# Kernel tuning notes

Hardware: AMD Instinct MI355X
Metric: run time of the kernel (lower is better)

The kernel has to match this reference:

```python
import jax, jax.numpy as jnp
import numpy as np
from jax import lax

B_CAPS, C_CAPS, K, STRIDE, ITERS = 32, 32, 3, 2, 3
BATCH, WIN = 8, 14
W_OUT = (WIN - K) // STRIDE + 1  # 6
CWW = C_CAPS * W_OUT * W_OUT     # 1152
LOG_2PI = float(np.log(2.0 * np.pi))


def setup_inputs() -> dict:
    key = jax.random.key(0)
    k1, k2, k3, k4, k5 = jax.random.split(key, 5)
    return {
        "poses": jax.random.normal(k1, (BATCH, B_CAPS, WIN, WIN, 16), jnp.float32),
        "activations": jax.random.uniform(k2, (BATCH, B_CAPS, WIN, WIN), jnp.float32),
        "lambda_": jnp.ones((), jnp.float32),
        "W": jax.random.normal(k3, (B_CAPS, K, K, C_CAPS, 4, 4), jnp.float32),
        "beta_v": jax.random.normal(k4, (1, CWW, 1), jnp.float32),
        "beta_a": jax.random.normal(k5, (1, CWW), jnp.float32),
    }


def reference(poses, activations, lambda_, W, beta_v, beta_a):
    b, B, win = poses.shape[0], poses.shape[1], poses.shape[2]
    C = W.shape[3]
    w = (win - K) // STRIDE + 1
    Bkk, Cww = B * K * K, C * w * w

    pose = poses.reshape(b, 16, B, win, win).transpose(0, 2, 3, 4, 1)

    # im2col patch extraction (vectorized): rows[i,k] = stride*i + k
    rows = ((jnp.arange(w) * STRIDE)[:, None] + jnp.arange(K)).reshape(-1)  # (w*K,)
    p = jnp.take(pose, rows, axis=2).reshape(b, B, w, K, win, 16)
    p = jnp.take(p, rows, axis=4).reshape(b, B, w, K, w, K, 16)
    patches = p.transpose(0, 1, 3, 5, 6, 2, 4)          # (b,B,K,K,16,wi,wj)
    # faithful reproduction of torch's view (b,B,K,K,16,ww)->(b,B,K,K,1,w,w,4,4)
    patches = patches.reshape(b, B, K, K, w, w, 4, 4)

    # votes: broadcast 4x4 matmul W @ pose-patch
    votes = jnp.einsum('sxyzij,bsxyuvjk->bsxyzuvik', W, patches)
    votes = votes.reshape(b, Bkk, Cww, 16)

    # activation patches, tiled over C (coordinate_add=False branch)
    a = jnp.take(activations, rows, axis=2).reshape(b, B, w, K, win)
    a = jnp.take(a, rows, axis=4).reshape(b, B, w, K, w, K)
    a = a.transpose(0, 1, 3, 5, 2, 4).reshape(b, Bkk, 1, w * w)
    act = jnp.broadcast_to(a, (b, Bkk, C, w * w)).reshape(b, Bkk, Cww)

    # EM routing
    R = jnp.ones((b, Bkk, Cww), votes.dtype) / Cww
    for i in range(ITERS + 1):
        Ra = (R * act)[..., None]                        # (b,Bkk,Cww,1)
        sum_R = Ra.sum(1)                                # (b,Cww,1)
        mu = ((Ra * votes).sum(1) / sum_R)[:, None]      # (b,1,Cww,16)
        sigma_sq = (Ra * (votes - mu) ** 2).sum(1) / sum_R  # (b,Cww,16)
        if i != ITERS:
            mu_d = lax.stop_gradient(mu)
            ss_d = lax.stop_gradient(sigma_sq)[:, None]  # (b,1,Cww,16)
            V_d = lax.stop_gradient(votes)
            a_d = lax.stop_gradient(act)
            log_p = -0.5 * (V_d - mu_d) ** 2 / ss_d - 0.5 * jnp.log(ss_d) - 0.5 * LOG_2PI
            ap = a_d * jnp.exp(log_p).sum(-1)            # (b,Bkk,Cww)
            R = ap / ap.sum(-1, keepdims=True)
        else:
            cost = (beta_v + jnp.log(sigma_sq)) * sum_R  # (b,Cww,16)
            a_out = jax.nn.sigmoid(lambda_ * (beta_a - cost.sum(2)))  # (b,Cww)

    return (mu.reshape(b, C, w, w, 16), a_out.reshape(b, C, w, w))
```

## Files before the change

### kernel.cpp

```cpp
#include <hip/hip_runtime.h>
#include <hip/hip_bf16.h>

#define NB   8
#define NM   288
#define NN   1152
#define NUV  36
#define ND   16

#define OFF_P    0
#define SZ_P     (NB*NUV*NM*ND)
#define OFF_WT   (OFF_P + SZ_P)
#define SZ_WT    (32*NM*ND)
#define OFF_ACT  (OFF_WT + SZ_WT)
#define SZ_ACT   (NB*NUV*NM)
#define OFF_L    (OFF_ACT + SZ_ACT)
#define SZ_L     (NB*NN*NM)
#define OFF_LSE  (OFF_L + SZ_L)
#define SZ_LSE   (NB*NM)
#define OFF_FLAG (OFF_LSE + SZ_LSE)
#define OFF_LT   (OFF_FLAG + 16)
#define SZ_LT    (NB*NM*NN)

#define HALF_LOG_2PI 0.9189385332046727f
#define LOG_NN       7.049254841255839f
#define NEG_BIG      (-1.0e30f)

__device__ __forceinline__ float ldin(const void* p, int i, int f32) {
    return f32 ? ((const float*)p)[i]
               : __bfloat162float(((const __hip_bfloat16*)p)[i]);
}

__device__ __forceinline__ unsigned short bfbits(float f) {
    __hip_bfloat16 h = __float2bfloat16(f);
    return __builtin_bit_cast(unsigned short, h);
}

__device__ __forceinline__ float dot2bf(unsigned a, unsigned b, float c) {
    float d;
    asm("v_dot2_f32_bf16 %0, %1, %2, %3" : "=v"(d) : "v"(a), "v"(b), "v"(c));
    return d;
}

__global__ void detect_kernel(const unsigned short* __restrict__ poses_u16,
                              int* __restrict__ flag) {
    if (blockIdx.x == 0 && threadIdx.x == 0) {
        int wild = 0;
        for (int i = 0; i < 64; ++i) {
            int ex = (poses_u16[i] >> 7) & 0xFF;
            if (ex >= 133) ++wild;
        }
        *flag = (wild >= 4) ? 1 : 0;
    }
}

__global__ __launch_bounds__(256) void prep_kernel(
    const void* __restrict__ poses, const void* __restrict__ acts,
    const void* __restrict__ Wb, __hip_bfloat16* __restrict__ P,
    __hip_bfloat16* __restrict__ Wt, float* __restrict__ A36,
    const int* __restrict__ flagp)
{
    const int f32 = *flagp;
    const int blk = blockIdx.x;
    const int tid = threadIdx.x;
    if (blk < 256) {
        __shared__ float ps[16 * 196];
        __shared__ float asld[196];
        const int b = blk >> 5, s = blk & 31;
        for (int e = tid; e < 16 * 196; e += 256) {
            int c = e / 196, hw = e % 196;
            ps[e] = ldin(poses, ((b * 16 + c) * 32 + s) * 196 + hw, f32);
        }
        for (int e = tid; e < 196; e += 256)
            asld[e] = ldin(acts, (b * 32 + s) * 196 + e, f32);
        __syncthreads();
        for (int o2 = tid; o2 < 648; o2 += 256) {
            int row = o2 >> 1, half = o2 & 1;
            int uv = row / 9, xy = row % 9;
            int u = uv / 6, vv2 = uv % 6;
            int x = xy / 3, y = xy % 3;
            unsigned pk[4];
#pragma unroll
            for (int h = 0; h < 4; ++h) {
                unsigned lohi[2];
#pragma unroll
                for (int e = 0; e < 2; ++e) {
                    int kj = half * 8 + h * 2 + e;
                    int k = kj >> 2, j = kj & 3;
                    int idx = u * 96 + vv2 * 16 + j * 4 + k;
                    int c = idx / 36, rem = idx % 36;
                    int wi = rem / 6, wj = rem % 6;
                    lohi[e] = bfbits(ps[c * 196 + (2 * wi + x) * 14 + (2 * wj + y)]);
                }
                pk[h] = lohi[0] | (lohi[1] << 16);
            }
            *((uint4*)(P + (((size_t)((b * 36 + uv) * 288 + s * 9 + xy)) << 4) + half * 8)) =
                make_uint4(pk[0], pk[1], pk[2], pk[3]);
        }
        for (int o = tid; o < 324; o += 256) {
            int uv = o / 9, xy = o % 9;
            int u = uv / 6, vv2 = uv % 6;
            int x = xy / 3, y = xy % 3;
            A36[(b * 36 + uv) * 288 + s * 9 + xy] =
                __logf(asld[(2 * u + x) * 14 + (2 * vv2 + y)]);
        }
    } else {
        int idx = (blk - 256) * 256 + tid;
        int z = idx / 288, m = idx % 288;
        unsigned pk[8];
#pragma unroll
        for (int h = 0; h < 8; ++h) {
            unsigned lo = bfbits(ldin(Wb, m * 512 + z * 16 + 2 * h, f32));
            unsigned hi = bfbits(ldin(Wb, m * 512 + z * 16 + 2 * h + 1, f32));
            pk[h] = lo | (hi << 16);
        }
        uint4* dst = (uint4*)(Wt + idx * 16);
        dst[0] = make_uint4(pk[0], pk[1], pk[2], pk[3]);
        dst[1] = make_uint4(pk[4], pk[5], pk[6], pk[7]);
    }
}

__global__ __launch_bounds__(288, 4) void em_iter(
    const unsigned short* __restrict__ wsP, const unsigned short* __restrict__ wsWt,
    const float* __restrict__ wsA, float* __restrict__ wsL,
    float* __restrict__ wsLT, const float* __restrict__ wsLSE,
    const void* __restrict__ beta_v,
    const void* __restrict__ beta_a,
    const void* __restrict__ lambda_,
    void* __restrict__ outv, const int* __restrict__ flagp, int iter)
{
    __shared__ float red[NM * 17];
    __shared__ float Mhw[9];
    __shared__ float paru[NM];
    __shared__ float parv[NM];
    __shared__ float paruW[18];
    __shared__ float mul[16], nhil[16], ltl[16], ssl[16];

    const int tid = threadIdx.x;
    const int B   = blockIdx.x;
    const int rr  = B & 255;
    const int z   = rr >> 3;
    const int g   = ((B >> 8) << 3) | (rr & 7);
    const int b   = g / NUV;
    const int uv  = g % NUV;
    const int n   = z * NUV + uv;
    const int bn  = b * NN + n;

    const uint4* Wq = (const uint4*)(wsWt + ((z * NM + tid) << 4));
    const uint4* Pq = (const uint4*)(wsP + ((g * NM + tid) << 4));
    uint4 wq0 = Wq[0], wq1 = Wq[1];
    uint4 pq0 = Pq[0], pq1 = Pq[1];
    const float lact = wsA[g * NM + tid];
    float t;
    if (iter == 0) t = lact - LOG_NN;
    else t = wsL[(size_t)bn * NM + tid] - wsLSE[b * NM + tid] + lact;
    t = fmaxf(t, NEG_BIG);

    float mhw = t;
#pragma unroll
    for (int off = 1; off < 32; off <<= 1)
        mhw = fmaxf(mhw, __shfl_xor(mhw, off, 32));
    const float w = __expf(t - mhw);
    if ((tid & 31) == 0) Mhw[tid >> 5] = mhw;

    unsigned Wa[4] = {wq0.x, wq0.z, wq1.x, wq1.z};
    unsigned Wb_[4] = {wq0.y, wq0.w, wq1.y, wq1.w};
    unsigned Pa[4] = {pq0.x, pq0.z, pq1.x, pq1.z};
    unsigned Pb[4] = {pq0.y, pq0.w, pq1.y, pq1.w};
    float v[16];
#pragma unroll
    for (int i = 0; i < 4; ++i)
#pragma unroll
        for (int k = 0; k < 4; ++k)
            v[i * 4 + k] = dot2bf(Wa[i], Pa[k], dot2bf(Wb_[i], Pb[k], 0.f));

#pragma unroll
    for (int dd = 0; dd < 16; ++dd) red[tid * 17 + dd] = v[dd];
    red[tid * 17 + 16] = w;
    __syncthreads();

    {
        const int d = tid & 15, c = tid >> 4;
        const float* base = &red[(c << 4) * 17];
        float s1 = 0.f, s2 = 0.f, sw = 0.f;
#pragma unroll
        for (int q = 0; q < 16; ++q) {
            float ww = base[q * 17 + 16];
            float vv = base[q * 17 + d];
            float t1 = ww * vv;
            s1 += t1; s2 += t1 * vv; sw += ww;
        }
        paru[d * 18 + c] = s1;
        parv[d * 18 + c] = s2;
        if (d == 0) paruW[c] = sw;
    }
    __syncthreads();

    float M_f = NEG_BIG, sW_f = 0.f;
    if (tid < 16) {
        float M = Mhw[0];
#pragma unroll
        for (int h = 1; h < 9; ++h) M = fmaxf(M, Mhw[h]);
        float sW = 0.f, S1 = 0.f, S2 = 0.f;
#pragma unroll
        for (int c = 0; c < 18; ++c) {
            float sc = __expf(Mhw[c >> 1] - M);
            sW += paruW[c] * sc;
            S1 += paru[tid * 18 + c] * sc;
            S2 += parv[tid * 18 + c] * sc;
        }
        float mu = S1 / sW;
        float q2 = S2 / sW;
        float ss = fmaxf(q2 - mu * mu, 1e-30f);
        mul[tid]  = mu;
        ssl[tid]  = ss;
        nhil[tid] = -0.5f / ss;
        ltl[tid]  = -0.5f * __logf(ss) - HALF_LOG_2PI;
        M_f = M; sW_f = sW;
    }
    __syncthreads();

    if (iter < 3) {
        float lp[16];
        float M = NEG_BIG;
#pragma unroll
        for (int dd = 0; dd < 16; ++dd) {
            float df = v[dd] - mul[dd];
            lp[dd] = df * df * nhil[dd] + ltl[dd];
            M = fmaxf(M, lp[dd]);
        }
        float s = 0.f;
#pragma unroll
        for (int dd = 0; dd < 16; ++dd) s += __expf(lp[dd] - M);
        float ell = lact + M + __logf(s);
        wsL[(size_t)bn * NM + tid] = ell;
        wsLT[((size_t)b * NM + tid) * NN + n] = ell;
    } else {
        const int f32 = *flagp;
        if (tid < 16) {
            if (f32) ((float*)outv)[(bn << 4) + tid] = mul[tid];
            else ((__hip_bfloat16*)outv)[(bn << 4) + tid] = __float2bfloat16(mul[tid]);
        }
        if (tid == 0) {
            float sumR = __expf(M_f) * sW_f;
            float bv = ldin(beta_v, n, f32);
            float c = 0.f;
#pragma unroll
            for (int dd = 0; dd < 16; ++dd) c += bv + __logf(ssl[dd]);
            c *= sumR;
            float lam = ldin(lambda_, 0, f32);
            float ba  = ldin(beta_a, n, f32);
            float ao  = 1.f / (1.f + __expf(-(lam * (ba - c))));
            int oi = NB * NN * ND + bn;
            if (f32) ((float*)outv)[oi] = ao;
            else ((__hip_bfloat16*)outv)[oi] = __float2bfloat16(ao);
        }
    }
}

__global__ __launch_bounds__(256) void lse_kernel(const float* __restrict__ LT,
                                                  float* __restrict__ LSE)
{
    const int row  = blockIdx.x * 4 + (threadIdx.x >> 6);
    const int lane = threadIdx.x & 63;
    const float* base = LT + (size_t)row * NN + lane;
    float vv[18];
    float mx = NEG_BIG;
#pragma unroll
    for (int i = 0; i < 18; ++i) { vv[i] = base[i * 64]; mx = fmaxf(mx, vv[i]); }
#pragma unroll
    for (int off = 1; off < 64; off <<= 1) mx = fmaxf(mx, __shfl_xor(mx, off));
    float s = 0.f;
#pragma unroll
    for (int i = 0; i < 18; ++i) s += __expf(vv[i] - mx);
#pragma unroll
    for (int off = 1; off < 64; off <<= 1) s += __shfl_xor(s, off);
    if (lane == 0) LSE[row] = mx + __logf(s);
}

extern "C" void kernel_launch(void* const* d_in, const int* in_sizes, int n_in,
                              void* d_out, int out_size, void* d_ws, size_t ws_size,
                              hipStream_t stream)
{
    const void* poses = d_in[0];
    const void* acts  = d_in[1];
    const void* lam   = d_in[2];
    const void* Wb    = d_in[3];
    const void* bv    = d_in[4];
    const void* ba    = d_in[5];

    float* ws  = (float*)d_ws;
    __hip_bfloat16* P  = (__hip_bfloat16*)(ws + OFF_P);
    __hip_bfloat16* Wt = (__hip_bfloat16*)(ws + OFF_WT);
    float* A36 = ws + OFF_ACT;
    float* L   = ws + OFF_L;
    float* LSE = ws + OFF_LSE;
    int*  flag = (int*)(ws + OFF_FLAG);
    float* LT  = ws + OFF_LT;

    detect_kernel<<<1, 64, 0, stream>>>((const unsigned short*)poses, flag);

    prep_kernel<<<292, 256, 0, stream>>>(poses, acts, Wb, P, Wt, A36, flag);

    for (int it = 0; it < 4; ++it) {
        em_iter<<<NB * NN, 288, 0, stream>>>((const unsigned short*)P,
                                             (const unsigned short*)Wt,
                                             A36, L, LT, LSE, bv, ba, lam,
                                             d_out, flag, it);
        if (it < 3) {
            lse_kernel<<<576, 256, 0, stream>>>(LT, LSE);
        }
    }
}
```

Baseline: 230.4 us.

## Replace transposed log-likelihood copy with two-stage partial log-sum-exp over L

The routing kernel no longer writes a second, transposed copy of the log-likelihoods (a strided scatter over NN). The normalizer is instead computed in two passes: one kernel reads L in its natural layout with coalesced accesses and produces per-chunk max and sum, and a small kernel merges the 36 partials per row. This removes an uncoalesced write of the full 8x1152x288 tensor on each iteration, at the cost of one extra kernel launch per iteration and a small partial buffer.

Result: no change. 231.7 us (+0.6%).

```diff
diff --git a/kernel.cpp b/kernel.cpp
--- a/kernel.cpp
+++ b/kernel.cpp
@@ -18,8 +18,10 @@
 #define OFF_LSE  (OFF_L + SZ_L)
 #define SZ_LSE   (NB*NM)
 #define OFF_FLAG (OFF_LSE + SZ_LSE)
-#define OFF_LT   (OFF_FLAG + 16)
-#define SZ_LT    (NB*NM*NN)
+#define OFF_PM   (OFF_FLAG + 16)
+#define SZ_PM    (NB*NUV*NM)
+#define OFF_PS   (OFF_PM + SZ_PM)
+#define SZ_PS    (NB*NUV*NM)
 
 #define HALF_LOG_2PI 0.9189385332046727f
 #define LOG_NN       7.049254841255839f
@@ -122,7 +124,7 @@
 __global__ __launch_bounds__(288, 4) void em_iter(
     const unsigned short* __restrict__ wsP, const unsigned short* __restrict__ wsWt,
     const float* __restrict__ wsA, float* __restrict__ wsL,
-    float* __restrict__ wsLT, const float* __restrict__ wsLSE,
+    const float* __restrict__ wsLSE,
     const void* __restrict__ beta_v,
     const void* __restrict__ beta_a,
     const void* __restrict__ lambda_,
@@ -162,10 +164,10 @@
     const float w = __expf(t - mhw);
     if ((tid & 31) == 0) Mhw[tid >> 5] = mhw;
 
-    unsigned Wa[4] = {wq0.x, wq0.z, wq1.x, wq1.z};
+    unsigned Wa[4]  = {wq0.x, wq0.z, wq1.x, wq1.z};
     unsigned Wb_[4] = {wq0.y, wq0.w, wq1.y, wq1.w};
-    unsigned Pa[4] = {pq0.x, pq0.z, pq1.x, pq1.z};
-    unsigned Pb[4] = {pq0.y, pq0.w, pq1.y, pq1.w};
+    unsigned Pa[4]  = {pq0.x, pq0.z, pq1.x, pq1.z};
+    unsigned Pb[4]  = {pq0.y, pq0.w, pq1.y, pq1.w};
     float v[16];
 #pragma unroll
     for (int i = 0; i < 4; ++i)
@@ -231,9 +233,7 @@
         float s = 0.f;
 #pragma unroll
         for (int dd = 0; dd < 16; ++dd) s += __expf(lp[dd] - M);
-        float ell = lact + M + __logf(s);
-        wsL[(size_t)bn * NM + tid] = ell;
-        wsLT[((size_t)b * NM + tid) * NN + n] = ell;
+        wsL[(size_t)bn * NM + tid] = lact + M + __logf(s);
     } else {
         const int f32 = *flagp;
         if (tid < 16) {
@@ -257,24 +257,41 @@
     }
 }
 
-__global__ __launch_bounds__(256) void lse_kernel(const float* __restrict__ LT,
-                                                  float* __restrict__ LSE)
-{
-    const int row  = blockIdx.x * 4 + (threadIdx.x >> 6);
-    const int lane = threadIdx.x & 63;
-    const float* base = LT + (size_t)row * NN + lane;
-    float vv[18];
+__global__ __launch_bounds__(288) void lse1_kernel(const float* __restrict__ L,
+                                                   float* __restrict__ PM,
+                                                   float* __restrict__ PS)
+{
+    const int tid = threadIdx.x;
+    const int blk = blockIdx.x;
+    const int b = blk / NUV;
+    const int c = blk % NUV;
+    const float* base = L + ((size_t)b * NN + c * 32) * NM + tid;
     float mx = NEG_BIG;
 #pragma unroll
-    for (int i = 0; i < 18; ++i) { vv[i] = base[i * 64]; mx = fmaxf(mx, vv[i]); }
-#pragma unroll
-    for (int off = 1; off < 64; off <<= 1) mx = fmaxf(mx, __shfl_xor(mx, off));
+    for (int r = 0; r < 32; ++r) mx = fmaxf(mx, base[r * NM]);
     float s = 0.f;
 #pragma unroll
-    for (int i = 0; i < 18; ++i) s += __expf(vv[i] - mx);
-#pragma unroll
-    for (int off = 1; off < 64; off <<= 1) s += __shfl_xor(s, off);
-    if (lane == 0) LSE[row] = mx + __logf(s);
+    for (int r = 0; r < 32; ++r) s += __expf(base[r * NM] - mx);
+    PM[blk * NM + tid] = mx;
+    PS[blk * NM + tid] = s;
+}
+
+__global__ void lse2_kernel(const float* __restrict__ PM,
+                            const float* __restrict__ PS,
+                            float* __restrict__ LSE)
+{
+    int t = blockIdx.x * 256 + threadIdx.x;
+    if (t >= NB * NM) return;
+    int b = t / NM, m = t % NM;
+    const float* pm = PM + (size_t)b * NUV * NM + m;
+    const float* ps = PS + (size_t)b * NUV * NM + m;
+    float mx = NEG_BIG;
+#pragma unroll
+    for (int cc = 0; cc < NUV; ++cc) mx = fmaxf(mx, pm[cc * NM]);
+    float s = 0.f;
+#pragma unroll
+    for (int cc = 0; cc < NUV; ++cc) s += ps[cc * NM] * __expf(pm[cc * NM] - mx);
+    LSE[t] = mx + __logf(s);
 }
 
 extern "C" void kernel_launch(void* const* d_in, const int* in_sizes, int n_in,
@@ -295,7 +312,8 @@
     float* L   = ws + OFF_L;
     float* LSE = ws + OFF_LSE;
     int*  flag = (int*)(ws + OFF_FLAG);
-    float* LT  = ws + OFF_LT;
+    float* PM  = ws + OFF_PM;
+    float* PS  = ws + OFF_PS;
 
     detect_kernel<<<1, 64, 0, stream>>>((const unsigned short*)poses, flag);
 
@@ -304,10 +322,11 @@
     for (int it = 0; it < 4; ++it) {
         em_iter<<<NB * NN, 288, 0, stream>>>((const unsigned short*)P,
                                              (const unsigned short*)Wt,
-                                             A36, L, LT, LSE, bv, ba, lam,
+                                             A36, L, LSE, bv, ba, lam,
                                              d_out, flag, it);
         if (it < 3) {
-            lse_kernel<<<576, 256, 0, stream>>>(LT, LSE);
-        }
-    }
-}
+            lse1_kernel<<<NB * NUV, 288, 0, stream>>>(L, PM, PS);
+            lse2_kernel<<<9, 256, 0, stream>>>(PM, PS, LSE);
+        }
+    }
+}
```

## Replace log-domain EM routing with linear-domain sums and drop transposed buffer

Applied to the files above, without the earlier changes.

Routing weights are now kept in the linear domain: em_iter writes a*sum(exp(log_p)) once, and a new sum_kernel computes per-(b,m) reciprocal sums, replacing the log-sum-exp path and its separate transposed LT buffer. This removes the max/exp rescaling and the strided transposed store, and cuts global traffic per iteration. The separate detect kernel is folded into prep_kernel, saving one launch. Linear-domain sums risk underflow or overflow, which the code handles only with small clamps.

After: 248.6 us. 7.9% more time.

```diff
diff --git a/kernel.cpp b/kernel.cpp
--- a/kernel.cpp
+++ b/kernel.cpp
@@ -13,16 +13,13 @@
 #define SZ_WT    (32*NM*ND)
 #define OFF_ACT  (OFF_WT + SZ_WT)
 #define SZ_ACT   (NB*NUV*NM)
-#define OFF_L    (OFF_ACT + SZ_ACT)
-#define SZ_L     (NB*NN*NM)
-#define OFF_LSE  (OFF_L + SZ_L)
-#define SZ_LSE   (NB*NM)
-#define OFF_FLAG (OFF_LSE + SZ_LSE)
-#define OFF_LT   (OFF_FLAG + 16)
-#define SZ_LT    (NB*NM*NN)
+#define OFF_PA   (OFF_ACT + SZ_ACT)
+#define SZ_PA    (NB*NN*NM)
+#define OFF_RS   (OFF_PA + SZ_PA)
+#define SZ_RS    (NB*NM)
+#define OFF_FLAG (OFF_RS + SZ_RS)
 
 #define HALF_LOG_2PI 0.9189385332046727f
-#define LOG_NN       7.049254841255839f
 #define NEG_BIG      (-1.0e30f)
 
 __device__ __forceinline__ float ldin(const void* p, int i, int f32) {
@@ -41,27 +38,32 @@
     return d;
 }
 
-__global__ void detect_kernel(const unsigned short* __restrict__ poses_u16,
-                              int* __restrict__ flag) {
-    if (blockIdx.x == 0 && threadIdx.x == 0) {
-        int wild = 0;
-        for (int i = 0; i < 64; ++i) {
-            int ex = (poses_u16[i] >> 7) & 0xFF;
-            if (ex >= 133) ++wild;
-        }
-        *flag = (wild >= 4) ? 1 : 0;
-    }
+__device__ __forceinline__ int sniff(const unsigned short* u16) {
+    int wild = 0;
+    for (int i = 0; i < 64; ++i) {
+        int ex = (u16[i] >> 7) & 0xFF;
+        if (ex >= 133) ++wild;
+    }
+    return (wild >= 4) ? 1 : 0;
 }
 
 __global__ __launch_bounds__(256) void prep_kernel(
     const void* __restrict__ poses, const void* __restrict__ acts,
     const void* __restrict__ Wb, __hip_bfloat16* __restrict__ P,
     __hip_bfloat16* __restrict__ Wt, float* __restrict__ A36,
-    const int* __restrict__ flagp)
-{
-    const int f32 = *flagp;
+    int* __restrict__ flagw)
+{
     const int blk = blockIdx.x;
     const int tid = threadIdx.x;
+    __shared__ int lflag;
+    if (tid == 0) {
+        int f = sniff((const unsigned short*)poses);
+        lflag = f;
+        if (blk == 0) *flagw = f;
+    }
+    __syncthreads();
+    const int f32 = lflag;
+
     if (blk < 256) {
         __shared__ float ps[16 * 196];
         __shared__ float asld[196];
@@ -101,7 +103,7 @@
             int u = uv / 6, vv2 = uv % 6;
             int x = xy / 3, y = xy % 3;
             A36[(b * 36 + uv) * 288 + s * 9 + xy] =
-                __logf(asld[(2 * u + x) * 14 + (2 * vv2 + y)]);
+                asld[(2 * u + x) * 14 + (2 * vv2 + y)];
         }
     } else {
         int idx = (blk - 256) * 256 + tid;
@@ -121,15 +123,14 @@
 
 __global__ __launch_bounds__(288, 4) void em_iter(
     const unsigned short* __restrict__ wsP, const unsigned short* __restrict__ wsWt,
-    const float* __restrict__ wsA, float* __restrict__ wsL,
-    float* __restrict__ wsLT, const float* __restrict__ wsLSE,
+    const float* __restrict__ wsA, float* __restrict__ wsPA,
+    const float* __restrict__ wsRS,
     const void* __restrict__ beta_v,
     const void* __restrict__ beta_a,
     const void* __restrict__ lambda_,
     void* __restrict__ outv, const int* __restrict__ flagp, int iter)
 {
     __shared__ float red[NM * 17];
-    __shared__ float Mhw[9];
     __shared__ float paru[NM];
     __shared__ float parv[NM];
     __shared__ float paruW[18];
@@ -149,23 +150,16 @@
     const uint4* Pq = (const uint4*)(wsP + ((g * NM + tid) << 4));
     uint4 wq0 = Wq[0], wq1 = Wq[1];
     uint4 pq0 = Pq[0], pq1 = Pq[1];
-    const float lact = wsA[g * NM + tid];
-    float t;
-    if (iter == 0) t = lact - LOG_NN;
-    else t = wsL[(size_t)bn * NM + tid] - wsLSE[b * NM + tid] + lact;
-    t = fmaxf(t, NEG_BIG);
-
-    float mhw = t;
-#pragma unroll
-    for (int off = 1; off < 32; off <<= 1)
-        mhw = fmaxf(mhw, __shfl_xor(mhw, off, 32));
-    const float w = __expf(t - mhw);
-    if ((tid & 31) == 0) Mhw[tid >> 5] = mhw;
-
-    unsigned Wa[4] = {wq0.x, wq0.z, wq1.x, wq1.z};
+    const float act = wsA[g * NM + tid];
+
+    float Ra;
+    if (iter == 0) Ra = act;
+    else Ra = act * wsPA[(size_t)bn * NM + tid] * wsRS[b * NM + tid];
+
+    unsigned Wa[4]  = {wq0.x, wq0.z, wq1.x, wq1.z};
     unsigned Wb_[4] = {wq0.y, wq0.w, wq1.y, wq1.w};
-    unsigned Pa[4] = {pq0.x, pq0.z, pq1.x, pq1.z};
-    unsigned Pb[4] = {pq0.y, pq0.w, pq1.y, pq1.w};
+    unsigned Pa[4]  = {pq0.x, pq0.z, pq1.x, pq1.z};
+    unsigned Pb[4]  = {pq0.y, pq0.w, pq1.y, pq1.w};
     float v[16];
 #pragma unroll
     for (int i = 0; i < 4; ++i)
@@ -175,7 +169,7 @@
 
 #pragma unroll
     for (int dd = 0; dd < 16; ++dd) red[tid * 17 + dd] = v[dd];
-    red[tid * 17 + 16] = w;
+    red[tid * 17 + 16] = Ra;
     __syncthreads();
 
     {
@@ -195,45 +189,35 @@
     }
     __syncthreads();
 
-    float M_f = NEG_BIG, sW_f = 0.f;
+    float sW_f = 0.f;
     if (tid < 16) {
-        float M = Mhw[0];
-#pragma unroll
-        for (int h = 1; h < 9; ++h) M = fmaxf(M, Mhw[h]);
         float sW = 0.f, S1 = 0.f, S2 = 0.f;
 #pragma unroll
         for (int c = 0; c < 18; ++c) {
-            float sc = __expf(Mhw[c >> 1] - M);
-            sW += paruW[c] * sc;
-            S1 += paru[tid * 18 + c] * sc;
-            S2 += parv[tid * 18 + c] * sc;
-        }
+            sW += paruW[c];
+            S1 += paru[tid * 18 + c];
+            S2 += parv[tid * 18 + c];
+        }
+        sW = fmaxf(sW, 1e-37f);
         float mu = S1 / sW;
         float q2 = S2 / sW;
         float ss = fmaxf(q2 - mu * mu, 1e-30f);
         mul[tid]  = mu;
         ssl[tid]  = ss;
         nhil[tid] = -0.5f / ss;
-        ltl[tid]  = -0.5f * __logf(ss) - HALF_LOG_2PI;
-        M_f = M; sW_f = sW;
+        ltl[tid]  = fmaf(-0.5f, __logf(ss), -HALF_LOG_2PI);
+        sW_f = sW;
     }
     __syncthreads();
 
     if (iter < 3) {
-        float lp[16];
-        float M = NEG_BIG;
+        float s = 0.f;
 #pragma unroll
         for (int dd = 0; dd < 16; ++dd) {
             float df = v[dd] - mul[dd];
-            lp[dd] = df * df * nhil[dd] + ltl[dd];
-            M = fmaxf(M, lp[dd]);
-        }
-        float s = 0.f;
-#pragma unroll
-        for (int dd = 0; dd < 16; ++dd) s += __expf(lp[dd] - M);
-        float ell = lact + M + __logf(s);
-        wsL[(size_t)bn * NM + tid] = ell;
-        wsLT[((size_t)b * NM + tid) * NN + n] = ell;
+            s += __expf(fmaf(df * df, nhil[dd], ltl[dd]));
+        }
+        wsPA[(size_t)bn * NM + tid] = fmaxf(act * s, 1e-30f);
     } else {
         const int f32 = *flagp;
         if (tid < 16) {
@@ -241,7 +225,7 @@
             else ((__hip_bfloat16*)outv)[(bn << 4) + tid] = __float2bfloat16(mul[tid]);
         }
         if (tid == 0) {
-            float sumR = __expf(M_f) * sW_f;
+            float sumR = sW_f;
             float bv = ldin(beta_v, n, f32);
             float c = 0.f;
 #pragma unroll
@@ -257,24 +241,26 @@
     }
 }
 
-__global__ __launch_bounds__(256) void lse_kernel(const float* __restrict__ LT,
-                                                  float* __restrict__ LSE)
-{
-    const int row  = blockIdx.x * 4 + (threadIdx.x >> 6);
-    const int lane = threadIdx.x & 63;
-    const float* base = LT + (size_t)row * NN + lane;
-    float vv[18];
-    float mx = NEG_BIG;
-#pragma unroll
-    for (int i = 0; i < 18; ++i) { vv[i] = base[i * 64]; mx = fmaxf(mx, vv[i]); }
-#pragma unroll
-    for (int off = 1; off < 64; off <<= 1) mx = fmaxf(mx, __shfl_xor(mx, off));
+__global__ __launch_bounds__(256) void sum_kernel(const float* __restrict__ PA,
+                                                  float* __restrict__ RS)
+{
+    __shared__ float red[16][17];
+    const int blk = blockIdx.x;
+    const int b  = blk / 18, mt = blk % 18;
+    const int n16 = threadIdx.x >> 4, m16 = threadIdx.x & 15;
+    const int m = mt * 16 + m16;
+    const float* base = PA + (size_t)b * NN * NM + m;
     float s = 0.f;
 #pragma unroll
-    for (int i = 0; i < 18; ++i) s += __expf(vv[i] - mx);
-#pragma unroll
-    for (int off = 1; off < 64; off <<= 1) s += __shfl_xor(s, off);
-    if (lane == 0) LSE[row] = mx + __logf(s);
+    for (int i = 0; i < 72; ++i) s += base[(size_t)(n16 + 16 * i) * NM];
+    red[n16][m16] = s;
+    __syncthreads();
+    if (threadIdx.x < 16) {
+        float t = 0.f;
+#pragma unroll
+        for (int q = 0; q < 16; ++q) t += red[q][threadIdx.x];
+        RS[b * NM + mt * 16 + threadIdx.x] = 1.0f / t;
+    }
 }
 
 extern "C" void kernel_launch(void* const* d_in, const int* in_sizes, int n_in,
@@ -292,22 +278,19 @@
     __hip_bfloat16* P  = (__hip_bfloat16*)(ws + OFF_P);
     __hip_bfloat16* Wt = (__hip_bfloat16*)(ws + OFF_WT);
     float* A36 = ws + OFF_ACT;
-    float* L   = ws + OFF_L;
-    float* LSE = ws + OFF_LSE;
+    float* PA  = ws + OFF_PA;
+    float* RS  = ws + OFF_RS;
     int*  flag = (int*)(ws + OFF_FLAG);
-    float* LT  = ws + OFF_LT;
-
-    detect_kernel<<<1, 64, 0, stream>>>((const unsigned short*)poses, flag);
 
     prep_kernel<<<292, 256, 0, stream>>>(poses, acts, Wb, P, Wt, A36, flag);
 
     for (int it = 0; it < 4; ++it) {
         em_iter<<<NB * NN, 288, 0, stream>>>((const unsigned short*)P,
                                              (const unsigned short*)Wt,
-                                             A36, L, LT, LSE, bv, ba, lam,
+                                             A36, PA, RS, bv, ba, lam,
                                              d_out, flag, it);
         if (it < 3) {
-            lse_kernel<<<576, 256, 0, stream>>>(LT, LSE);
-        }
-    }
-}
+            sum_kernel<<<NB * 18, 256, 0, stream>>>(PA, RS);
+        }
+    }
+}
```
